# Performance work log

Hardware: AMD Instinct MI355X
Metric: run time of the kernel (lower is better)

The kernel has to match this reference:

```python
import jax, jax.numpy as jnp
import numpy as np

EMPTY, TRUE, FALSE = 0.0, 1.0, 2.0  # MemoryVal ternary encoding

B = 2048          # batch
IN_BITS = 4096    # raw input bits
N_IN, N_ST, N_OUT = 2048, 1024, 1024
K = 14            # bits (connections) per neuron -> memory_size = 2**K
M = 2 ** K


def setup_inputs() -> dict:
    key = jax.random.key(0)
    ks = jax.random.split(key, 8)
    return {
        "input_bits": jax.random.randint(ks[0], (B, IN_BITS), 0, 2, dtype=jnp.int32),
        "state_bits": jax.random.randint(ks[1], (B, N_ST), 0, 2, dtype=jnp.int32),
        "in_conn": jax.random.randint(ks[2], (N_IN, K), 0, IN_BITS, dtype=jnp.int32),
        "in_mem": jax.random.randint(ks[3], (N_IN, M), 0, 3).astype(jnp.float32),
        "st_conn": jax.random.randint(ks[4], (N_ST, K), 0, N_IN + N_ST, dtype=jnp.int32),
        "st_mem": jax.random.randint(ks[5], (N_ST, M), 0, 3).astype(jnp.float32),
        "out_conn": jax.random.randint(ks[6], (N_OUT, K), 0, N_IN + N_ST, dtype=jnp.int32),
        "out_mem": jax.random.randint(ks[7], (N_OUT, M), 0, 3).astype(jnp.float32),
    }


def _ram_layer(bits, conn, mem):
    """bits: [B, T] 0/1; conn: [N, K] indices into T; mem: [N, 2**K] ternary."""
    k = conn.shape[1]
    g = bits[:, conn].astype(jnp.int32)                      # [B, N, K] gathered local bits
    w = (2 ** jnp.arange(k - 1, -1, -1)).astype(jnp.int32)   # MSB-first packing (matches _get_desired_bits)
    addr = jnp.sum(g * w, axis=-1)                           # [B, N] memory addresses
    vals = mem[jnp.arange(mem.shape[0])[None, :], addr]      # [B, N] per-neuron LUT lookup
    return jnp.where(vals == TRUE, 1.0, 0.0).astype(jnp.float32)  # neuron fires iff TRUE


def reference(input_bits, state_bits, in_conn, in_mem, st_conn, st_mem, out_conn, out_mem):
    h_in = _ram_layer(input_bits, in_conn, in_mem)                          # [B, N_IN]
    s_inp = jnp.concatenate([h_in, state_bits.astype(h_in.dtype)], axis=1)  # [B, N_IN+N_ST]
    s_out = _ram_layer(s_inp, st_conn, st_mem)                              # [B, N_ST]
    o_inp = jnp.concatenate([h_in, s_out], axis=1)                          # [B, N_IN+N_ST]
    return _ram_layer(o_inp, out_conn, out_mem)                             # [B, N_OUT]
```

## Files before the change

kernel.cpp:

```cpp
#include <hip/hip_runtime.h>
#include <stdint.h>

#define BATCH   2048
#define IN_BITS 4096
#define N_IN    2048
#define N_ST    1024
#define N_OUT   1024
#define KBITS   14
#define MW      512
#define SROW    96

#define GS  524288

typedef float f32x4 __attribute__((ext_vector_type(4)));
typedef int   i32x4 __attribute__((ext_vector_type(4)));

__device__ __forceinline__ void emit1f(uint32_t* __restrict__ d, long i,
                                       int lane, f32x4 v) {
    unsigned long long b0 = __ballot(v[0] == 1.0f);
    unsigned long long b1 = __ballot(v[1] == 1.0f);
    unsigned long long b2 = __ballot(v[2] == 1.0f);
    unsigned long long b3 = __ballot(v[3] == 1.0f);
    if (lane < 8) {
        unsigned long long bj = (lane & 4) ? ((lane & 2) ? b3 : b2)
                                           : ((lane & 2) ? b1 : b0);
        uint32_t w = (lane & 1) ? (uint32_t)(bj >> 32) : (uint32_t)bj;
        d[((i >> 6) << 3) + lane] = w;
    }
}
__device__ __forceinline__ void emit1i(uint32_t* __restrict__ d, long i,
                                       int lane, i32x4 v) {
    unsigned long long b0 = __ballot(v[0] == 1);
    unsigned long long b1 = __ballot(v[1] == 1);
    unsigned long long b2 = __ballot(v[2] == 1);
    unsigned long long b3 = __ballot(v[3] == 1);
    if (lane < 8) {
        unsigned long long bj = (lane & 4) ? ((lane & 2) ? b3 : b2)
                                           : ((lane & 2) ? b1 : b0);
        uint32_t w = (lane & 1) ? (uint32_t)(bj >> 32) : (uint32_t)bj;
        d[((i >> 6) << 3) + lane] = w;
    }
}

__global__ __launch_bounds__(256) void pack_all(
    const float* __restrict__ im, const float* __restrict__ sm,
    const float* __restrict__ om, const int* __restrict__ ib,
    const int* __restrict__ sb,
    uint32_t* __restrict__ im_p, uint32_t* __restrict__ sm_p,
    uint32_t* __restrict__ om_p, uint32_t* __restrict__ bits1,
    uint32_t* __restrict__ buf_s) {
    const long t = blockIdx.x * 256 + threadIdx.x;
    const int lane = threadIdx.x & 63;

    f32x4 va[8], vb[8];
#pragma unroll
    for (int u = 0; u < 8; ++u) va[u] = ((const f32x4*)im)[(long)u * GS + t];
#pragma unroll
    for (int u = 0; u < 8; ++u) vb[u] = ((const f32x4*)im)[(long)(u + 8) * GS + t];
#pragma unroll
    for (int u = 0; u < 8; ++u) emit1f(im_p, (long)u * GS + t, lane, va[u]);
#pragma unroll
    for (int u = 0; u < 8; ++u) va[u] = ((const f32x4*)sm)[(long)u * GS + t];
#pragma unroll
    for (int u = 0; u < 8; ++u) emit1f(im_p, (long)(u + 8) * GS + t, lane, vb[u]);
#pragma unroll
    for (int u = 0; u < 8; ++u) vb[u] = ((const f32x4*)om)[(long)u * GS + t];
#pragma unroll
    for (int u = 0; u < 8; ++u) emit1f(sm_p, (long)u * GS + t, lane, va[u]);
    i32x4 wi[4];
#pragma unroll
    for (int u = 0; u < 4; ++u) wi[u] = ((const i32x4*)ib)[(long)u * GS + t];
    i32x4 wst = ((const i32x4*)sb)[t];
#pragma unroll
    for (int u = 0; u < 8; ++u) emit1f(om_p, (long)u * GS + t, lane, vb[u]);
#pragma unroll
    for (int u = 0; u < 4; ++u) emit1i(bits1, (long)u * GS + t, lane, wi[u]);
    {
        uint32_t nib = (uint32_t)(wst[0] == 1) | ((uint32_t)(wst[1] == 1) << 1) |
                       ((uint32_t)(wst[2] == 1) << 2) | ((uint32_t)(wst[3] == 1) << 3);
        uint32_t w = nib << (4 * (lane & 7));
        w |= __shfl_xor(w, 1, 64);
        w |= __shfl_xor(w, 2, 64);
        w |= __shfl_xor(w, 4, 64);
        if ((lane & 7) == 0) {
            long g = t >> 3;
            buf_s[(g >> 5) * SROW + 64 + (int)(g & 31)] = w;
        }
    }
}

template <int SRCW, int MODE>
__global__ __launch_bounds__(256) void ram_layer_t(const uint32_t* __restrict__ src,
                                                   const int* __restrict__ conn,
                                                   const uint32_t* __restrict__ memp,
                                                   uint32_t* __restrict__ dst0,
                                                   uint32_t* __restrict__ dst1,
                                                   float* __restrict__ fout) {
    constexpr int LSTR = SRCW + 1;
    __shared__ uint32_t lds[64 * LSTR];
    const int tid = threadIdx.x;
    const int b0 = blockIdx.y * 64;
    {
        const uint4* g = (const uint4*)(src + (long)b0 * SRCW);
        constexpr int NQ = 64 * SRCW / 4;
#pragma unroll
        for (int i = tid; i < NQ; i += 256) {
            uint4 v = g[i];
            int r = i / (SRCW / 4);
            int w = (i - r * (SRCW / 4)) * 4;
            uint32_t* p = &lds[r * LSTR + w];
            p[0] = v.x; p[1] = v.y; p[2] = v.z; p[3] = v.w;
        }
    }
    __syncthreads();
    const int lane = tid & 63;
    const int wave = __builtin_amdgcn_readfirstlane(tid >> 6);
    const int nw0 = blockIdx.x * 64 + wave * 16;
    const long b = b0 + lane;
    const uint32_t* row = lds + lane * LSTR;
    uint32_t acc = 0;
#pragma unroll 2
    for (int j = 0; j < 16; ++j) {
        const int n = nw0 + j;
        const int* cp = conn + n * KBITS;
        uint32_t addr = 0;
#pragma unroll
        for (int k = 0; k < KBITS; ++k) {
            int idx = cp[k];
            int wd, sh;
            if (SRCW == 128) {
                wd = ((idx >> 5) & ~7) | ((idx & 3) << 1) | ((idx >> 7) & 1);
                sh = (idx >> 2) & 31;
            } else {
                wd = idx >> 5;
                sh = idx & 31;
            }
            addr = (addr << 1) | ((row[wd] >> sh) & 1u);
        }
        uint32_t mw = ((addr >> 5) & ~7u) | ((addr & 3u) << 1) | ((addr >> 7) & 1u);
        uint32_t bit = (memp[(long)n * MW + mw] >> ((addr >> 2) & 31u)) & 1u;
        if (MODE == 2) fout[b * N_OUT + n] = (float)bit;
        else           acc |= bit << j;
    }
    if (MODE != 2) {
        const int woff = (MODE == 0 ? 0 : 64) + (nw0 >> 5);
        const int half = (nw0 >> 4) & 1;
        ((ushort*)(dst0 + b * SROW + woff))[half] = (ushort)acc;
        if (MODE == 0)
            ((ushort*)(dst1 + b * SROW + woff))[half] = (ushort)acc;
    }
}

extern "C" void kernel_launch(void* const* d_in, const int* in_sizes, int n_in,
                              void* d_out, int out_size, void* d_ws, size_t ws_size,
                              hipStream_t stream) {
    const int*   input_bits = (const int*)d_in[0];
    const int*   state_bits = (const int*)d_in[1];
    const int*   in_conn    = (const int*)d_in[2];
    const float* in_mem     = (const float*)d_in[3];
    const int*   st_conn    = (const int*)d_in[4];
    const float* st_mem     = (const float*)d_in[5];
    const int*   out_conn   = (const int*)d_in[6];
    const float* out_mem    = (const float*)d_in[7];
    float*       out        = (float*)d_out;

    char* ws = (char*)d_ws;
    uint32_t* bits1 = (uint32_t*)(ws);
    uint32_t* buf_s = (uint32_t*)(ws + 1048576);
    uint32_t* buf_o = (uint32_t*)(ws + 1048576 + 786432);
    uint32_t* im_p  = (uint32_t*)(ws + 1048576 + 2 * 786432);
    uint32_t* sm_p  = (uint32_t*)(ws + 1048576 + 2 * 786432 + 4194304);
    uint32_t* om_p  = (uint32_t*)(ws + 1048576 + 2 * 786432 + 4194304 + 2097152);

    pack_all<<<2048, 256, 0, stream>>>(in_mem, st_mem, out_mem,
                                       input_bits, state_bits,
                                       im_p, sm_p, om_p, bits1, buf_s);
    ram_layer_t<128, 0><<<dim3(N_IN / 64, BATCH / 64), 256, 0, stream>>>(
        bits1, in_conn, im_p, buf_s, buf_o, nullptr);
    ram_layer_t<SROW, 1><<<dim3(N_ST / 64, BATCH / 64), 256, 0, stream>>>(
        buf_s, st_conn, sm_p, buf_o, nullptr, nullptr);
    ram_layer_t<SROW, 2><<<dim3(N_OUT / 64, BATCH / 64), 256, 0, stream>>>(
        buf_o, out_conn, om_p, nullptr, nullptr, out);
}
```

Before: 374.5 us.

## Drop memory-table bit packing and gather directly from float LUTs

Removes the pre-pass that read all three float memory tables and packed them to bitmaps, and instead has each RAM layer read the float entry at the computed address directly. This aims to avoid streaming the full tables once per call, at the cost of scattered 4-byte gathers over much larger per-neuron rows with worse cache locality. It also vectorizes the final float output stores and raises the neuron loop unroll.

```diff
diff --git a/kernel.cpp b/kernel.cpp
--- a/kernel.cpp
+++ b/kernel.cpp
@@ -7,7 +7,7 @@
 #define N_ST    1024
 #define N_OUT   1024
 #define KBITS   14
-#define MW      512
+#define MROW    16384
 #define SROW    96
 
 #define GS  524288
@@ -15,19 +15,7 @@
 typedef float f32x4 __attribute__((ext_vector_type(4)));
 typedef int   i32x4 __attribute__((ext_vector_type(4)));
 
-__device__ __forceinline__ void emit1f(uint32_t* __restrict__ d, long i,
-                                       int lane, f32x4 v) {
-    unsigned long long b0 = __ballot(v[0] == 1.0f);
-    unsigned long long b1 = __ballot(v[1] == 1.0f);
-    unsigned long long b2 = __ballot(v[2] == 1.0f);
-    unsigned long long b3 = __ballot(v[3] == 1.0f);
-    if (lane < 8) {
-        unsigned long long bj = (lane & 4) ? ((lane & 2) ? b3 : b2)
-                                           : ((lane & 2) ? b1 : b0);
-        uint32_t w = (lane & 1) ? (uint32_t)(bj >> 32) : (uint32_t)bj;
-        d[((i >> 6) << 3) + lane] = w;
-    }
-}
+
 __device__ __forceinline__ void emit1i(uint32_t* __restrict__ d, long i,
                                        int lane, i32x4 v) {
     unsigned long long b0 = __ballot(v[0] == 1);
@@ -42,57 +30,34 @@
     }
 }
 
-__global__ __launch_bounds__(256) void pack_all(
-    const float* __restrict__ im, const float* __restrict__ sm,
-    const float* __restrict__ om, const int* __restrict__ ib,
-    const int* __restrict__ sb,
-    uint32_t* __restrict__ im_p, uint32_t* __restrict__ sm_p,
-    uint32_t* __restrict__ om_p, uint32_t* __restrict__ bits1,
-    uint32_t* __restrict__ buf_s) {
+__global__ __launch_bounds__(256) void pack_in_st(const int* __restrict__ ib,
+                                                  const int* __restrict__ sb,
+                                                  uint32_t* __restrict__ bits1,
+                                                  uint32_t* __restrict__ buf_s) {
     const long t = blockIdx.x * 256 + threadIdx.x;
     const int lane = threadIdx.x & 63;
-
-    f32x4 va[8], vb[8];
-#pragma unroll
-    for (int u = 0; u < 8; ++u) va[u] = ((const f32x4*)im)[(long)u * GS + t];
-#pragma unroll
-    for (int u = 0; u < 8; ++u) vb[u] = ((const f32x4*)im)[(long)(u + 8) * GS + t];
-#pragma unroll
-    for (int u = 0; u < 8; ++u) emit1f(im_p, (long)u * GS + t, lane, va[u]);
-#pragma unroll
-    for (int u = 0; u < 8; ++u) va[u] = ((const f32x4*)sm)[(long)u * GS + t];
-#pragma unroll
-    for (int u = 0; u < 8; ++u) emit1f(im_p, (long)(u + 8) * GS + t, lane, vb[u]);
-#pragma unroll
-    for (int u = 0; u < 8; ++u) vb[u] = ((const f32x4*)om)[(long)u * GS + t];
-#pragma unroll
-    for (int u = 0; u < 8; ++u) emit1f(sm_p, (long)u * GS + t, lane, va[u]);
     i32x4 wi[4];
 #pragma unroll
     for (int u = 0; u < 4; ++u) wi[u] = ((const i32x4*)ib)[(long)u * GS + t];
     i32x4 wst = ((const i32x4*)sb)[t];
 #pragma unroll
-    for (int u = 0; u < 8; ++u) emit1f(om_p, (long)u * GS + t, lane, vb[u]);
-#pragma unroll
     for (int u = 0; u < 4; ++u) emit1i(bits1, (long)u * GS + t, lane, wi[u]);
-    {
-        uint32_t nib = (uint32_t)(wst[0] == 1) | ((uint32_t)(wst[1] == 1) << 1) |
-                       ((uint32_t)(wst[2] == 1) << 2) | ((uint32_t)(wst[3] == 1) << 3);
-        uint32_t w = nib << (4 * (lane & 7));
-        w |= __shfl_xor(w, 1, 64);
-        w |= __shfl_xor(w, 2, 64);
-        w |= __shfl_xor(w, 4, 64);
-        if ((lane & 7) == 0) {
-            long g = t >> 3;
-            buf_s[(g >> 5) * SROW + 64 + (int)(g & 31)] = w;
-        }
+    uint32_t nib = (uint32_t)(wst[0] == 1) | ((uint32_t)(wst[1] == 1) << 1) |
+                   ((uint32_t)(wst[2] == 1) << 2) | ((uint32_t)(wst[3] == 1) << 3);
+    uint32_t w = nib << (4 * (lane & 7));
+    w |= __shfl_xor(w, 1, 64);
+    w |= __shfl_xor(w, 2, 64);
+    w |= __shfl_xor(w, 4, 64);
+    if ((lane & 7) == 0) {
+        long g = t >> 3;
+        buf_s[(g >> 5) * SROW + 64 + (int)(g & 31)] = w;
     }
 }
 
 template <int SRCW, int MODE>
-__global__ __launch_bounds__(256) void ram_layer_t(const uint32_t* __restrict__ src,
+__global__ __launch_bounds__(256) void ram_layer_f(const uint32_t* __restrict__ src,
                                                    const int* __restrict__ conn,
-                                                   const uint32_t* __restrict__ memp,
+                                                   const float* __restrict__ memf,
                                                    uint32_t* __restrict__ dst0,
                                                    uint32_t* __restrict__ dst1,
                                                    float* __restrict__ fout) {
@@ -119,7 +84,7 @@
     const long b = b0 + lane;
     const uint32_t* row = lds + lane * LSTR;
     uint32_t acc = 0;
-#pragma unroll 2
+#pragma unroll 4
     for (int j = 0; j < 16; ++j) {
         const int n = nw0 + j;
         const int* cp = conn + n * KBITS;
@@ -137,12 +102,19 @@
             }
             addr = (addr << 1) | ((row[wd] >> sh) & 1u);
         }
-        uint32_t mw = ((addr >> 5) & ~7u) | ((addr & 3u) << 1) | ((addr >> 7) & 1u);
-        uint32_t bit = (memp[(long)n * MW + mw] >> ((addr >> 2) & 31u)) & 1u;
-        if (MODE == 2) fout[b * N_OUT + n] = (float)bit;
-        else           acc |= bit << j;
+        float v = memf[(long)n * MROW + addr];
+        acc |= ((v == 1.0f) ? 1u : 0u) << j;
     }
-    if (MODE != 2) {
+    if (MODE == 2) {
+        float* op = fout + b * N_OUT + nw0;
+#pragma unroll
+        for (int q = 0; q < 4; ++q) {
+            f32x4 f;
+#pragma unroll
+            for (int e = 0; e < 4; ++e) f[e] = (float)((acc >> (q * 4 + e)) & 1u);
+            ((f32x4*)op)[q] = f;
+        }
+    } else {
         const int woff = (MODE == 0 ? 0 : 64) + (nw0 >> 5);
         const int half = (nw0 >> 4) & 1;
         ((ushort*)(dst0 + b * SROW + woff))[half] = (ushort)acc;
@@ -168,17 +140,12 @@
     uint32_t* bits1 = (uint32_t*)(ws);
     uint32_t* buf_s = (uint32_t*)(ws + 1048576);
     uint32_t* buf_o = (uint32_t*)(ws + 1048576 + 786432);
-    uint32_t* im_p  = (uint32_t*)(ws + 1048576 + 2 * 786432);
-    uint32_t* sm_p  = (uint32_t*)(ws + 1048576 + 2 * 786432 + 4194304);
-    uint32_t* om_p  = (uint32_t*)(ws + 1048576 + 2 * 786432 + 4194304 + 2097152);
 
-    pack_all<<<2048, 256, 0, stream>>>(in_mem, st_mem, out_mem,
-                                       input_bits, state_bits,
-                                       im_p, sm_p, om_p, bits1, buf_s);
-    ram_layer_t<128, 0><<<dim3(N_IN / 64, BATCH / 64), 256, 0, stream>>>(
-        bits1, in_conn, im_p, buf_s, buf_o, nullptr);
-    ram_layer_t<SROW, 1><<<dim3(N_ST / 64, BATCH / 64), 256, 0, stream>>>(
-        buf_s, st_conn, sm_p, buf_o, nullptr, nullptr);
-    ram_layer_t<SROW, 2><<<dim3(N_OUT / 64, BATCH / 64), 256, 0, stream>>>(
-        buf_o, out_conn, om_p, nullptr, nullptr, out);
+    pack_in_st<<<2048, 256, 0, stream>>>(input_bits, state_bits, bits1, buf_s);
+    ram_layer_f<128, 0><<<dim3(N_IN / 64, BATCH / 64), 256, 0, stream>>>(
+        bits1, in_conn, in_mem, buf_s, buf_o, nullptr);
+    ram_layer_f<SROW, 1><<<dim3(N_ST / 64, BATCH / 64), 256, 0, stream>>>(
+        buf_s, st_conn, st_mem, buf_o, nullptr, nullptr);
+    ram_layer_f<SROW, 2><<<dim3(N_OUT / 64, BATCH / 64), 256, 0, stream>>>(
+        buf_o, out_conn, out_mem, nullptr, nullptr, out);
 }
```

After: 357.6 us. 1.05x faster.

## Stream LUT packing through LDS with double-buffered direct global-to-LDS loads

Applied to the files above, without the earlier changes.

The packing kernel is rewritten so each wave handles contiguous 4 KB chunks of the memory tables and input bits. It uses global_load_lds to copy them straight into a per-wave double-buffered LDS region, so loads overlap with the ballot-and-store packing of the previous chunk. This replaces the old large register-staged strided loads and is meant to raise achieved bandwidth on the heavily memory-bound pack step. It adds LDS use and a hand-written vmcnt wait whose count may also be affected by the interleaved global stores.

```diff
diff --git a/kernel.cpp b/kernel.cpp
--- a/kernel.cpp
+++ b/kernel.cpp
@@ -10,12 +10,11 @@
 #define MW      512
 #define SROW    96
 
-#define GS  524288
-
 typedef float f32x4 __attribute__((ext_vector_type(4)));
 typedef int   i32x4 __attribute__((ext_vector_type(4)));
 
-__device__ __forceinline__ void emit1f(uint32_t* __restrict__ d, long i,
+
+__device__ __forceinline__ void emit1f(uint32_t* __restrict__ d, long gi,
                                        int lane, f32x4 v) {
     unsigned long long b0 = __ballot(v[0] == 1.0f);
     unsigned long long b1 = __ballot(v[1] == 1.0f);
@@ -25,10 +24,10 @@
         unsigned long long bj = (lane & 4) ? ((lane & 2) ? b3 : b2)
                                            : ((lane & 2) ? b1 : b0);
         uint32_t w = (lane & 1) ? (uint32_t)(bj >> 32) : (uint32_t)bj;
-        d[((i >> 6) << 3) + lane] = w;
-    }
-}
-__device__ __forceinline__ void emit1i(uint32_t* __restrict__ d, long i,
+        d[((gi >> 6) << 3) + lane] = w;
+    }
+}
+__device__ __forceinline__ void emit1i(uint32_t* __restrict__ d, long gi,
                                        int lane, i32x4 v) {
     unsigned long long b0 = __ballot(v[0] == 1);
     unsigned long long b1 = __ballot(v[1] == 1);
@@ -38,53 +37,76 @@
         unsigned long long bj = (lane & 4) ? ((lane & 2) ? b3 : b2)
                                            : ((lane & 2) ? b1 : b0);
         uint32_t w = (lane & 1) ? (uint32_t)(bj >> 32) : (uint32_t)bj;
-        d[((i >> 6) << 3) + lane] = w;
-    }
-}
-
-__global__ __launch_bounds__(256) void pack_all(
-    const float* __restrict__ im, const float* __restrict__ sm,
-    const float* __restrict__ om, const int* __restrict__ ib,
+        d[((gi >> 6) << 3) + lane] = w;
+    }
+}
+
+__global__ __launch_bounds__(256) void pack_dma(
+    const uint32_t* __restrict__ im, const uint32_t* __restrict__ sm,
+    const uint32_t* __restrict__ om, const uint32_t* __restrict__ ib,
     const int* __restrict__ sb,
     uint32_t* __restrict__ im_p, uint32_t* __restrict__ sm_p,
     uint32_t* __restrict__ om_p, uint32_t* __restrict__ bits1,
     uint32_t* __restrict__ buf_s) {
-    const long t = blockIdx.x * 256 + threadIdx.x;
-    const int lane = threadIdx.x & 63;
-
-    f32x4 va[8], vb[8];
-#pragma unroll
-    for (int u = 0; u < 8; ++u) va[u] = ((const f32x4*)im)[(long)u * GS + t];
-#pragma unroll
-    for (int u = 0; u < 8; ++u) vb[u] = ((const f32x4*)im)[(long)(u + 8) * GS + t];
-#pragma unroll
-    for (int u = 0; u < 8; ++u) emit1f(im_p, (long)u * GS + t, lane, va[u]);
-#pragma unroll
-    for (int u = 0; u < 8; ++u) va[u] = ((const f32x4*)sm)[(long)u * GS + t];
-#pragma unroll
-    for (int u = 0; u < 8; ++u) emit1f(im_p, (long)(u + 8) * GS + t, lane, vb[u]);
-#pragma unroll
-    for (int u = 0; u < 8; ++u) vb[u] = ((const f32x4*)om)[(long)u * GS + t];
-#pragma unroll
-    for (int u = 0; u < 8; ++u) emit1f(sm_p, (long)u * GS + t, lane, va[u]);
-    i32x4 wi[4];
-#pragma unroll
-    for (int u = 0; u < 4; ++u) wi[u] = ((const i32x4*)ib)[(long)u * GS + t];
-    i32x4 wst = ((const i32x4*)sb)[t];
-#pragma unroll
-    for (int u = 0; u < 8; ++u) emit1f(om_p, (long)u * GS + t, lane, vb[u]);
-#pragma unroll
-    for (int u = 0; u < 4; ++u) emit1i(bits1, (long)u * GS + t, lane, wi[u]);
+    __shared__ uint32_t sbuf[4][2][1024];
+    const int tid  = threadIdx.x;
+    const int lane = tid & 63;
+    const int w    = tid >> 6;
+    const long slot = blockIdx.x * 4 + w;
+
+    const uint32_t* srcs[9] = { im, im, im, im, sm, sm, om, om, ib };
+    uint32_t*       dsts[9] = { im_p, im_p, im_p, im_p, sm_p, sm_p,
+                                om_p, om_p, bits1 };
+    const long      bats[9] = { slot, slot + 8192, slot + 16384, slot + 24576,
+                                slot, slot + 8192, slot, slot + 8192, slot };
+
+    auto issue = [&](int s, int pp) {
+        const uint32_t* tab = srcs[s];
+        const long base = bats[s] * 1024;
+#pragma unroll
+        for (int q = 0; q < 4; ++q)
+            __builtin_amdgcn_global_load_lds(
+                (const __attribute__((address_space(1))) uint32_t*)
+                    (tab + base + q * 256 + lane * 4),
+                (__attribute__((address_space(3))) uint32_t*)
+                    (&sbuf[w][pp][q * 256]),
+                16, 0, 0);
+    };
+
+    issue(0, 0);
+    issue(1, 1);
+#pragma unroll
+    for (int s = 0; s < 9; ++s) {
+        asm volatile("s_waitcnt vmcnt(4)" ::: "memory");
+        const int pp = s & 1;
+        const long b = bats[s];
+        uint32_t* d = dsts[s];
+#pragma unroll
+        for (int q = 0; q < 4; ++q) {
+            const long gi = b * 256 + q * 64 + lane;
+            if (s < 8) {
+                f32x4 v = *(const f32x4*)&sbuf[w][pp][q * 256 + lane * 4];
+                emit1f(d, gi, lane, v);
+            } else {
+                i32x4 v = *(const i32x4*)&sbuf[w][pp][q * 256 + lane * 4];
+                emit1i(d, gi, lane, v);
+            }
+        }
+        if (s + 2 < 9) issue(s + 2, pp);
+    }
+
     {
-        uint32_t nib = (uint32_t)(wst[0] == 1) | ((uint32_t)(wst[1] == 1) << 1) |
-                       ((uint32_t)(wst[2] == 1) << 2) | ((uint32_t)(wst[3] == 1) << 3);
-        uint32_t w = nib << (4 * (lane & 7));
-        w |= __shfl_xor(w, 1, 64);
-        w |= __shfl_xor(w, 2, 64);
-        w |= __shfl_xor(w, 4, 64);
+        const long t = (long)blockIdx.x * 256 + tid;
+        i32x4 v = ((const i32x4*)sb)[t];
+        uint32_t nib = (uint32_t)(v[0] == 1) | ((uint32_t)(v[1] == 1) << 1) |
+                       ((uint32_t)(v[2] == 1) << 2) | ((uint32_t)(v[3] == 1) << 3);
+        uint32_t wv = nib << (4 * (lane & 7));
+        wv |= __shfl_xor(wv, 1, 64);
+        wv |= __shfl_xor(wv, 2, 64);
+        wv |= __shfl_xor(wv, 4, 64);
         if ((lane & 7) == 0) {
             long g = t >> 3;
-            buf_s[(g >> 5) * SROW + 64 + (int)(g & 31)] = w;
+            buf_s[(g >> 5) * SROW + 64 + (int)(g & 31)] = wv;
         }
     }
 }
@@ -172,9 +194,10 @@
     uint32_t* sm_p  = (uint32_t*)(ws + 1048576 + 2 * 786432 + 4194304);
     uint32_t* om_p  = (uint32_t*)(ws + 1048576 + 2 * 786432 + 4194304 + 2097152);
 
-    pack_all<<<2048, 256, 0, stream>>>(in_mem, st_mem, out_mem,
-                                       input_bits, state_bits,
-                                       im_p, sm_p, om_p, bits1, buf_s);
+    pack_dma<<<2048, 256, 0, stream>>>(
+        (const uint32_t*)in_mem, (const uint32_t*)st_mem,
+        (const uint32_t*)out_mem, (const uint32_t*)input_bits, state_bits,
+        im_p, sm_p, om_p, bits1, buf_s);
     ram_layer_t<128, 0><<<dim3(N_IN / 64, BATCH / 64), 256, 0, stream>>>(
         bits1, in_conn, im_p, buf_s, buf_o, nullptr);
     ram_layer_t<SROW, 1><<<dim3(N_ST / 64, BATCH / 64), 256, 0, stream>>>(
```

Result: faster. 361.8 us (-3.4%).
